# Performance work log

Measured on AMD Instinct MI355X. Metric: run time of the kernel, lower is better.

The kernel has to match this reference:

```python
import jax, jax.numpy as jnp
import numpy as np

AGENT_RADIUS = 0.2
SAFETY_DIST = 0.1
_ang = np.linspace(0.0, 2.0 * np.pi, 8, endpoint=False)
OBSTACLES = np.stack([10.0 * np.cos(_ang), 10.0 * np.sin(_ang), 0.5 * np.ones(8)], axis=-1).astype(np.float32)  # (x, y, r)


def _qp_solve(p, G, h):
    """Exact solve of: min_z 0.5 z^T z + p^T z  s.t. G z <= h, z in R^2.
    Equivalent to QPFunction with Q=I. Enumerates KKT candidates over active
    sets of size 0, 1, 2 (closed form in 2D) and picks the feasible optimum.
    p: [2], G: [m,2], h: [m]."""
    m = G.shape[0]
    ii, jj = np.triu_indices(m, 1)
    # active set {} -> unconstrained minimizer
    z0 = -p[None, :]                                        # [1,2]
    # active set {i}: z = -p - lam*g_i, g_i.z = h_i
    gg = jnp.sum(G * G, axis=-1)                            # [m]
    lam1 = (-(G @ p) - h) / (gg + 1e-12)
    z1 = -p[None, :] - lam1[:, None] * G                    # [m,2]
    ok1 = lam1 >= -1e-8
    # active set {i,j}: z solves 2x2 system [g_i; g_j] z = [h_i; h_j]
    Gi, Gj = G[ii], G[jj]                                   # [P,2]
    hi, hj = h[ii], h[jj]
    det = Gi[:, 0] * Gj[:, 1] - Gi[:, 1] * Gj[:, 0]
    det_ok = jnp.abs(det) > 1e-9
    ds = jnp.where(det_ok, det, 1.0)
    zx = (hi * Gj[:, 1] - hj * Gi[:, 1]) / ds
    zy = (Gi[:, 0] * hj - Gj[:, 0] * hi) / ds
    z2 = jnp.stack([zx, zy], axis=-1)                       # [P,2]
    r = -(z2 + p[None, :])                                  # A^T lam = r
    lam_i = (Gj[:, 1] * r[:, 0] - Gj[:, 0] * r[:, 1]) / ds
    lam_j = (Gi[:, 0] * r[:, 1] - Gi[:, 1] * r[:, 0]) / ds
    ok2 = det_ok & (lam_i >= -1e-8) & (lam_j >= -1e-8)
    Z = jnp.concatenate([z0, z1, z2], axis=0)               # [K,2]
    ok = jnp.concatenate([jnp.ones((1,), bool), ok1, ok2], axis=0)
    tol = 1e-6 * (1.0 + jnp.abs(h))
    feas = jnp.all(Z @ G.T <= (h + tol)[None, :], axis=-1)  # [K]
    obj = 0.5 * jnp.sum(Z * Z, axis=-1) + Z @ p
    obj = jnp.where(ok & feas, obj, jnp.inf)
    return Z[jnp.argmin(obj)]


def _forward(x, mean, std, W1, b1, W21, b21, W31, b31, W22, b22, W32, b32):
    x0 = x * std + mean                                     # de-normalized state [B,8]
    hid = jax.nn.relu(x @ W1.T + b1)
    x31 = jax.nn.relu(hid @ W21.T + b21) @ W31.T + b31      # reference control p [B,2]
    x32 = 4.0 * jax.nn.sigmoid(jax.nn.relu(hid @ W22.T + b22) @ W32.T + b32)  # CBF penalties [B,2]
    px, py, theta, v = x0[:, 0], x0[:, 1], x0[:, 2], x0[:, 3]
    ox, oy, oth, ov = x0[:, 4], x0[:, 5], x0[:, 6], x0[:, 7]
    st, ct = jnp.sin(theta), jnp.cos(theta)
    vs, vc = v * st, v * ct
    obs = jnp.asarray(OBSTACLES, x.dtype)
    # static obstacle constraints, vectorized over the n_obs obstacles
    dx = px[:, None] - obs[None, :, 0]                      # [B,n_obs]
    dy = py[:, None] - obs[None, :, 1]
    R = AGENT_RADIUS + obs[:, 2] + SAFETY_DIST
    bar = dx * dx + dy * dy - (R * R)[None, :]
    bdot = 2.0 * dx * vc[:, None] + 2.0 * dy * vs[:, None]
    Lf2b = (2.0 * v * v)[:, None]
    u1 = -2.0 * dx * vs[:, None] + 2.0 * dy * vc[:, None]
    u2 = 2.0 * dx * ct[:, None] + 2.0 * dy * st[:, None]
    G_obs = -jnp.stack([u1, u2], axis=-1)                   # [B,n_obs,2]
    s0, s1 = x32[:, 0:1], x32[:, 1:2]
    h_obs = Lf2b + (s0 + s1) * bdot + (s0 * s1) * bar       # [B,n_obs]
    # opponent constraint
    Ro = 2.0 * AGENT_RADIUS + SAFETY_DIST
    dxo, dyo = px - ox, py - oy
    so, co = jnp.sin(oth), jnp.cos(oth)
    bar_o = dxo * dxo + dyo * dyo - Ro * Ro
    bdot_o = 2.0 * dxo * (vc - ov * co) + 2.0 * dyo * (vs - ov * so)
    Lf2b_o = 2.0 * (v * v + ov * ov + 2.0 * v * ov * jnp.cos(theta - oth))
    u1o = -2.0 * dxo * vs + 2.0 * dyo * vc
    u2o = 2.0 * dxo * ct + 2.0 * dyo * st
    G_opp = -jnp.stack([u1o, u2o], axis=-1)[:, None, :]     # [B,1,2]
    h_opp = (Lf2b_o + (x32[:, 0] + x32[:, 1]) * bdot_o + x32[:, 0] * x32[:, 1] * bar_o)[:, None]
    G = jnp.concatenate([G_obs, G_opp], axis=1)             # [B,m,2]
    h = jnp.concatenate([h_obs, h_opp], axis=1)             # [B,m]
    return jax.vmap(_qp_solve)(x31, G, h)                   # [B,2]


def setup_inputs() -> dict:
    key = jax.random.key(0)
    ks = jax.random.split(key, 6)
    B, nF, H1, H2 = 65536, 8, 256, 128

    def lin(k, o, i):
        k1, k2 = jax.random.split(k)
        W = jax.random.normal(k1, (o, i), jnp.float32) / np.float32(np.sqrt(i))
        b = jax.random.normal(k2, (o,), jnp.float32) * 0.01
        return W, b

    W1, b1 = lin(ks[0], H1, nF)
    W21, b21 = lin(ks[1], H2, H1)
    W31, b31 = lin(ks[2], 2, H2)
    W22, b22 = lin(ks[3], H2, H1)
    W32, b32 = lin(ks[4], 2, H2)
    x = jax.random.normal(ks[5], (B, nF), jnp.float32)
    return {"x": x, "mean": jnp.zeros((nF,), jnp.float32), "std": jnp.ones((nF,), jnp.float32),
            "W1": W1, "b1": b1, "W21": W21, "b21": b21, "W31": W31, "b31": b31,
            "W22": W22, "b22": b22, "W32": W32, "b32": b32, "sgn": 1}


def reference(x, mean, std, W1, b1, W21, b21, W31, b31, W22, b22, W32, b32, sgn):
    # sgn==1 / training path -> batched differentiable QP solve
    return _forward(x, mean, std, W1, b1, W21, b21, W31, b31, W22, b22, W32, b32)
```

## Files before the change

### kernel.cpp

```cpp
#include <hip/hip_runtime.h>
#include <math.h>


typedef unsigned int u32;
typedef unsigned long long u64;
typedef unsigned short u16;
typedef __attribute__((ext_vector_type(8))) short short8;
typedef __attribute__((ext_vector_type(4))) float f32x4;
typedef __attribute__((ext_vector_type(2))) float f32x2;
typedef __attribute__((ext_vector_type(4))) u32 u32x4;

union Frag { short8 v; u32 u[4]; u32x4 q; };

__device__ __forceinline__ u16 f2bf(float f) {
    union { float f; u32 i; } v; v.f = f;
    u32 b = v.i;
    return (u16)((b + 0x7fffu + ((b >> 16) & 1u)) >> 16);
}
__device__ __forceinline__ u32 packbf(float a, float b) {
    return (u32)f2bf(a) | ((u32)f2bf(b) << 16);
}

__device__ const float OBX[8] = { 10.f, 7.07106781186547524f, 6.123234e-16f, -7.07106781186547524f,
                                 -10.f, -7.07106781186547524f, -1.8369702e-15f, 7.07106781186547524f };
__device__ const float OBY[8] = { 0.f, 7.07106781186547524f, 10.f, 7.07106781186547524f,
                                  1.2246468e-15f, -7.07106781186547524f, -10.f, -7.07106781186547524f };

#define PI0_ 0x2111111100000000ULL
#define PI1_ 0x5544443333322222ULL
#define PI2_ 0x7665ULL
#define PJ0_ 0x3876543287654321ULL
#define PJ1_ 0x7687658765487654ULL
#define PJ2_ 0x8878ULL
__device__ __forceinline__ int unpack4(u64 w0, u64 w1, u64 w2, int t) {
    u64 w = (t < 16) ? w0 : (t < 32) ? w1 : w2;
    return (int)((w >> ((t & 15) * 4)) & 15);
}

__global__ __launch_bounds__(256)
void prep_kernel(const float* __restrict__ W21, const float* __restrict__ W22,
                 u32* __restrict__ ws)
{
    int idx  = blockIdx.x * 256 + threadIdx.x;
    int lane = idx & 63;
    int nt   = (idx >> 6) & 7;
    int ks   = (idx >> 9) & 7;
    int head = idx >> 12;
    const float* W = head ? W22 : W21;
    int n  = nt * 16 + (lane & 15);
    int k0 = ks * 32 + (lane >> 4) * 8;
    const float* s = W + n * 256 + k0;
    u32x4 o;
    o.x = packbf(s[0], s[1]);
    o.y = packbf(s[2], s[3]);
    o.z = packbf(s[4], s[5]);
    o.w = packbf(s[6], s[7]);
    ((u32x4*)ws)[idx] = o;
}

__global__ __launch_bounds__(256)
void gemm_kernel(const float* __restrict__ x,
                 const float* __restrict__ W1,
                 const float* __restrict__ b1,
                 const float* __restrict__ b21,
                 const float* __restrict__ W31,
                 const float* __restrict__ b31,
                 const float* __restrict__ b22,
                 const float* __restrict__ W32,
                 const float* __restrict__ b32,
                 const u32* __restrict__ wsB,
                 f32x4* __restrict__ ps, int Btot)
{
    const int tid  = threadIdx.x;
    const int wave = tid >> 6;
    const int lane = tid & 63;
    const int q    = lane >> 4;
    const int m    = lane & 15;
    const int blockRow = blockIdx.x * 128;
    const int waveRow  = blockRow + wave * 32;

    __shared__ float lds_p[128][4];

    float xf0[8], xf1[8];
    {
        int R0 = waveRow + m, R1 = waveRow + 16 + m;
        const float* xp0 = x + (R0 < Btot ? R0 : 0) * 8;
        const float* xp1 = x + (R1 < Btot ? R1 : 0) * 8;
        #pragma unroll
        for (int c = 0; c < 8; ++c) { xf0[c] = xp0[c]; xf1[c] = xp1[c]; }
    }

    const f32x4* W1v = (const f32x4*)W1;
    const f32x4* b1v = (const f32x4*)b1;

    #pragma unroll 1
    for (int head = 0; head < 2; ++head) {
        const u32x4* Bb = (const u32x4*)wsB + head * 4096 + lane;
        const float* b2 = head ? b22 : b21;
        const float* W3 = head ? W32 : W31;
        const float* b3 = head ? b32 : b31;

        f32x4 acc[2][8];
        #pragma unroll
        for (int mt = 0; mt < 2; ++mt)
            #pragma unroll
            for (int nt = 0; nt < 8; ++nt) acc[mt][nt] = (f32x4){0.f, 0.f, 0.f, 0.f};

        #pragma unroll 1
        for (int ks = 0; ks < 8; ++ks) {
            int kb = ks * 32 + q * 8;
            f32x4 bA = b1v[kb >> 2];
            f32x4 bB = b1v[(kb >> 2) + 1];
            Frag A0, A1;
            float h0[8], h1[8];
            #pragma unroll
            for (int j = 0; j < 8; ++j) {
                f32x4 wa = W1v[(kb + j) * 2];
                f32x4 wb = W1v[(kb + j) * 2 + 1];
                float bj = (j < 4) ? bA[j] : bB[j - 4];
                float a0 = bj, a1 = bj;
                a0 = fmaf(wa.x, xf0[0], a0); a1 = fmaf(wa.x, xf1[0], a1);
                a0 = fmaf(wa.y, xf0[1], a0); a1 = fmaf(wa.y, xf1[1], a1);
                a0 = fmaf(wa.z, xf0[2], a0); a1 = fmaf(wa.z, xf1[2], a1);
                a0 = fmaf(wa.w, xf0[3], a0); a1 = fmaf(wa.w, xf1[3], a1);
                a0 = fmaf(wb.x, xf0[4], a0); a1 = fmaf(wb.x, xf1[4], a1);
                a0 = fmaf(wb.y, xf0[5], a0); a1 = fmaf(wb.y, xf1[5], a1);
                a0 = fmaf(wb.z, xf0[6], a0); a1 = fmaf(wb.z, xf1[6], a1);
                a0 = fmaf(wb.w, xf0[7], a0); a1 = fmaf(wb.w, xf1[7], a1);
                h0[j] = fmaxf(a0, 0.f);
                h1[j] = fmaxf(a1, 0.f);
            }
            #pragma unroll
            for (int t = 0; t < 4; ++t) {
                A0.u[t] = packbf(h0[2 * t], h0[2 * t + 1]);
                A1.u[t] = packbf(h1[2 * t], h1[2 * t + 1]);
            }
            const u32x4* Bks = Bb + ks * 512;
            #pragma unroll
            for (int nt = 0; nt < 8; ++nt) {
                Frag Bf; Bf.q = Bks[nt * 64];
                acc[0][nt] = __builtin_amdgcn_mfma_f32_16x16x32_bf16(A0.v, Bf.v, acc[0][nt], 0, 0, 0);
                acc[1][nt] = __builtin_amdgcn_mfma_f32_16x16x32_bf16(A1.v, Bf.v, acc[1][nt], 0, 0, 0);
            }
        }

        float pr0[2][4], pr1[2][4];
        #pragma unroll
        for (int mt = 0; mt < 2; ++mt)
            #pragma unroll
            for (int rg = 0; rg < 4; ++rg) { pr0[mt][rg] = 0.f; pr1[mt][rg] = 0.f; }
        #pragma unroll
        for (int nt = 0; nt < 8; ++nt) {
            int col = nt * 16 + m;
            float b2c = b2[col];
            float w0c = W3[col];
            float w1c = W3[128 + col];
            #pragma unroll
            for (int mt = 0; mt < 2; ++mt) {
                #pragma unroll
                for (int rg = 0; rg < 4; ++rg) {
                    float rv = fmaxf(acc[mt][nt][rg] + b2c, 0.f);
                    pr0[mt][rg] = fmaf(rv, w0c, pr0[mt][rg]);
                    pr1[mt][rg] = fmaf(rv, w1c, pr1[mt][rg]);
                }
            }
        }
        #pragma unroll
        for (int mt = 0; mt < 2; ++mt) {
            #pragma unroll
            for (int rg = 0; rg < 4; ++rg) {
                float v0 = pr0[mt][rg], v1 = pr1[mt][rg];
                #pragma unroll
                for (int off = 1; off < 16; off <<= 1) {
                    v0 += __shfl_xor(v0, off, 64);
                    v1 += __shfl_xor(v1, off, 64);
                }
                pr0[mt][rg] = v0; pr1[mt][rg] = v1;
            }
        }
        if (m == 0) {
            #pragma unroll
            for (int mt = 0; mt < 2; ++mt) {
                #pragma unroll
                for (int rg = 0; rg < 4; ++rg) {
                    int row = wave * 32 + mt * 16 + q * 4 + rg;
                    float a0 = pr0[mt][rg] + b3[0];
                    float a1 = pr1[mt][rg] + b3[1];
                    if (head == 0) {
                        lds_p[row][0] = a0;
                        lds_p[row][1] = a1;
                    } else {
                        lds_p[row][2] = 4.f / (1.f + expf(-a0));
                        lds_p[row][3] = 4.f / (1.f + expf(-a1));
                    }
                }
            }
        }
    }
    __syncthreads();

    if (tid < 128) {
        int R = blockRow + tid;
        if (R < Btot) ps[R] = *(const f32x4*)lds_p[tid];
    }
}

__global__ __launch_bounds__(256)
void qp_kernel(const float* __restrict__ x,
               const float* __restrict__ meanp,
               const float* __restrict__ stdp,
               const f32x4* __restrict__ ps,
               float* __restrict__ out, int Btot)
{
    const int tid  = threadIdx.x;
    const int rq   = tid & 127;
    const int half = tid >> 7;
    const int blockRow = blockIdx.x * 128;
    const int R    = blockRow + rq;

    __shared__ f32x4 qC[9][128];
    __shared__ f32x4 res[128];

    f32x4 pv = ps[R < Btot ? R : 0];
    float p0 = pv.x, p1 = pv.y;

    if (half == 0) {
        float s0 = pv.z, s1 = pv.w;
        float xr[8];
        const float* xp = x + (R < Btot ? R : 0) * 8;
        #pragma unroll
        for (int c = 0; c < 8; ++c) xr[c] = fmaf(xp[c], stdp[c], meanp[c]);
        float px = xr[0], py = xr[1], th = xr[2], v = xr[3];
        float ox = xr[4], oy = xr[5], oth = xr[6], ov = xr[7];
        float st = sinf(th),  ct = cosf(th);
        float so = sinf(oth), co = cosf(oth);
        float vs = v * st, vc = v * ct;
        float sps = s0 + s1, ss = s0 * s1;
        float Lf2b = 2.f * v * v;
        #pragma unroll 1
        for (int k = 0; k < 8; ++k) {
            float dx = px - OBX[k], dy = py - OBY[k];
            float bar  = dx * dx + dy * dy - 0.64f;
            float bdot = 2.f * dx * vc + 2.f * dy * vs;
            float gx = 2.f * dx * vs - 2.f * dy * vc;
            float gy = -(2.f * dx * ct + 2.f * dy * st);
            float hk = Lf2b + sps * bdot + ss * bar;
            float ht = hk + 1e-6f * (1.f + fabsf(hk));
            qC[k][rq] = (f32x4){gx, gy, hk, ht};
        }
        {
            float dxo = px - ox, dyo = py - oy;
            float bar_o  = dxo * dxo + dyo * dyo - 0.25f;
            float bdot_o = 2.f * dxo * (vc - ov * co) + 2.f * dyo * (vs - ov * so);
            float Lf2b_o = 2.f * (v * v + ov * ov + 2.f * v * ov * cosf(th - oth));
            float gx = 2.f * dxo * vs - 2.f * dyo * vc;
            float gy = -(2.f * dxo * ct + 2.f * dyo * st);
            float hk = Lf2b_o + sps * bdot_o + ss * bar_o;
            float ht = hk + 1e-6f * (1.f + fabsf(hk));
            qC[8][rq] = (f32x4){gx, gy, hk, ht};
        }
    }
    __syncthreads();

    const f32x4 C0 = qC[0][rq], C1 = qC[1][rq], C2 = qC[2][rq];
    const f32x4 C3 = qC[3][rq], C4 = qC[4][rq], C5 = qC[5][rq];
    const f32x4 C6 = qC[6][rq], C7 = qC[7][rq], C8 = qC[8][rq];

    const int c0i = half ? 23 : 0;
    const int c1i = half ? 46 : 23;
    float bobj = INFINITY;
    float bzx = -p0, bzy = -p1;
    #pragma unroll 2
    for (int c = c0i; c < c1i; ++c) {
        float zx, zy;
        bool pre;
        if (c == 0) {
            zx = -p0; zy = -p1; pre = true;
        } else if (c <= 9) {
            f32x4 g = qC[c - 1][rq];
            float gg  = g.x * g.x + g.y * g.y;
            float lam = (-(g.x * p0 + g.y * p1) - g.z) / (gg + 1e-12f);
            zx = -p0 - lam * g.x;
            zy = -p1 - lam * g.y;
            pre = (lam >= -1e-8f);
        } else {
            int t = c - 10;
            int pi = unpack4(PI0_, PI1_, PI2_, t);
            int pj = unpack4(PJ0_, PJ1_, PJ2_, t);
            f32x4 gi = qC[pi][rq];
            f32x4 gj = qC[pj][rq];
            float det = gi.x * gj.y - gi.y * gj.x;
            bool dok = fabsf(det) > 1e-9f;
            float ds = dok ? det : 1.0f;
            float inv = 1.0f / ds;
            zx = (gi.z * gj.y - gj.z * gi.y) * inv;
            zy = (gi.x * gj.z - gj.x * gi.z) * inv;
            float rx = -(zx + p0), ry = -(zy + p1);
            float li = (gj.y * rx - gj.x * ry) * inv;
            float lj = (gi.x * ry - gi.y * rx) * inv;
            pre = dok && (li >= -1e-8f) && (lj >= -1e-8f);
        }
        bool ok = pre;
        ok = ok && (zx * C0.x + zy * C0.y <= C0.w);
        ok = ok && (zx * C1.x + zy * C1.y <= C1.w);
        ok = ok && (zx * C2.x + zy * C2.y <= C2.w);
        ok = ok && (zx * C3.x + zy * C3.y <= C3.w);
        ok = ok && (zx * C4.x + zy * C4.y <= C4.w);
        ok = ok && (zx * C5.x + zy * C5.y <= C5.w);
        ok = ok && (zx * C6.x + zy * C6.y <= C6.w);
        ok = ok && (zx * C7.x + zy * C7.y <= C7.w);
        ok = ok && (zx * C8.x + zy * C8.y <= C8.w);
        float obj = 0.5f * (zx * zx + zy * zy) + zx * p0 + zy * p1;
        if (ok && obj < bobj) { bobj = obj; bzx = zx; bzy = zy; }
    }

    if (half) {
        res[rq] = (f32x4){bobj, bzx, bzy, 0.f};
    }
    __syncthreads();
    if (!half) {
        f32x4 r = res[rq];
        if (r.x < bobj) { bzx = r.y; bzy = r.z; }
        if (R < Btot) {
            f32x2 o2; o2.x = bzx; o2.y = bzy;
            ((f32x2*)out)[R] = o2;
        }
    }
}

extern "C" void kernel_launch(void* const* d_in, const int* in_sizes, int n_in,
                              void* d_out, int out_size, void* d_ws, size_t ws_size,
                              hipStream_t stream) {
    const float* x    = (const float*)d_in[0];
    const float* mean = (const float*)d_in[1];
    const float* stdv = (const float*)d_in[2];
    const float* W1   = (const float*)d_in[3];
    const float* b1   = (const float*)d_in[4];
    const float* W21  = (const float*)d_in[5];
    const float* b21  = (const float*)d_in[6];
    const float* W31  = (const float*)d_in[7];
    const float* b31  = (const float*)d_in[8];
    const float* W22  = (const float*)d_in[9];
    const float* b22  = (const float*)d_in[10];
    const float* W32  = (const float*)d_in[11];
    const float* b32  = (const float*)d_in[12];
    int B = in_sizes[0] / 8;
    float* out = (float*)d_out;
    u32* ws = (u32*)d_ws;
    f32x4* ps = (f32x4*)(ws + 32768);

    hipLaunchKernelGGL(prep_kernel, dim3(32), dim3(256), 0, stream, W21, W22, ws);

    int blocks = (B + 127) / 128;
    hipLaunchKernelGGL(gemm_kernel, dim3(blocks), dim3(256), 0, stream,
                       x, W1, b1, b21, W31, b31, b22, W32, b32, ws, ps, B);
    hipLaunchKernelGGL(qp_kernel, dim3(blocks), dim3(256), 0, stream,
                       x, mean, stdv, ps, out, B);
}
```

Baseline: 128.6 us.

## Fuse both MLP heads into one K loop sharing layer-1 activations

Merges the two head passes into a single K loop, so the first-layer hidden activations are computed and packed to bf16 once and feed MFMAs for both heads. This removes the duplicated layer-1 FMA work and W1 loads. In exchange the accumulator count doubles to 64 f32x4 per lane, which raises VGPR/AGPR pressure and may cut occupancy. It also swaps the hand-written bf16 rounding for the HIP packed conversion intrinsic.

```diff
diff --git a/kernel.cpp b/kernel.cpp
--- a/kernel.cpp
+++ b/kernel.cpp
@@ -1,4 +1,5 @@
 #include <hip/hip_runtime.h>
+#include <hip/hip_bf16.h>
 #include <math.h>
 
 
@@ -12,13 +13,11 @@
 
 union Frag { short8 v; u32 u[4]; u32x4 q; };
 
-__device__ __forceinline__ u16 f2bf(float f) {
-    union { float f; u32 i; } v; v.f = f;
-    u32 b = v.i;
-    return (u16)((b + 0x7fffu + ((b >> 16) & 1u)) >> 16);
-}
 __device__ __forceinline__ u32 packbf(float a, float b) {
-    return (u32)f2bf(a) | ((u32)f2bf(b) << 16);
+    float2 f2; f2.x = a; f2.y = b;
+    __hip_bfloat162 h = __float22bfloat162_rn(f2);
+    union { __hip_bfloat162 h2; u32 u; } cv; cv.h2 = h;
+    return cv.u;
 }
 
 __device__ const float OBX[8] = { 10.f, 7.07106781186547524f, 6.123234e-16f, -7.07106781186547524f,
@@ -93,57 +92,64 @@
     const f32x4* W1v = (const f32x4*)W1;
     const f32x4* b1v = (const f32x4*)b1;
 
+    f32x4 acc[2][2][8];
+    #pragma unroll
+    for (int hd = 0; hd < 2; ++hd)
+        #pragma unroll
+        for (int mt = 0; mt < 2; ++mt)
+            #pragma unroll
+            for (int nt = 0; nt < 8; ++nt) acc[hd][mt][nt] = (f32x4){0.f, 0.f, 0.f, 0.f};
+
+    const u32x4* Bb = (const u32x4*)wsB + lane;
+
     #pragma unroll 1
-    for (int head = 0; head < 2; ++head) {
-        const u32x4* Bb = (const u32x4*)wsB + head * 4096 + lane;
-        const float* b2 = head ? b22 : b21;
-        const float* W3 = head ? W32 : W31;
-        const float* b3 = head ? b32 : b31;
-
-        f32x4 acc[2][8];
-        #pragma unroll
-        for (int mt = 0; mt < 2; ++mt)
-            #pragma unroll
-            for (int nt = 0; nt < 8; ++nt) acc[mt][nt] = (f32x4){0.f, 0.f, 0.f, 0.f};
-
-        #pragma unroll 1
-        for (int ks = 0; ks < 8; ++ks) {
-            int kb = ks * 32 + q * 8;
-            f32x4 bA = b1v[kb >> 2];
-            f32x4 bB = b1v[(kb >> 2) + 1];
-            Frag A0, A1;
-            float h0[8], h1[8];
-            #pragma unroll
-            for (int j = 0; j < 8; ++j) {
-                f32x4 wa = W1v[(kb + j) * 2];
-                f32x4 wb = W1v[(kb + j) * 2 + 1];
-                float bj = (j < 4) ? bA[j] : bB[j - 4];
-                float a0 = bj, a1 = bj;
-                a0 = fmaf(wa.x, xf0[0], a0); a1 = fmaf(wa.x, xf1[0], a1);
-                a0 = fmaf(wa.y, xf0[1], a0); a1 = fmaf(wa.y, xf1[1], a1);
-                a0 = fmaf(wa.z, xf0[2], a0); a1 = fmaf(wa.z, xf1[2], a1);
-                a0 = fmaf(wa.w, xf0[3], a0); a1 = fmaf(wa.w, xf1[3], a1);
-                a0 = fmaf(wb.x, xf0[4], a0); a1 = fmaf(wb.x, xf1[4], a1);
-                a0 = fmaf(wb.y, xf0[5], a0); a1 = fmaf(wb.y, xf1[5], a1);
-                a0 = fmaf(wb.z, xf0[6], a0); a1 = fmaf(wb.z, xf1[6], a1);
-                a0 = fmaf(wb.w, xf0[7], a0); a1 = fmaf(wb.w, xf1[7], a1);
-                h0[j] = fmaxf(a0, 0.f);
-                h1[j] = fmaxf(a1, 0.f);
-            }
-            #pragma unroll
-            for (int t = 0; t < 4; ++t) {
-                A0.u[t] = packbf(h0[2 * t], h0[2 * t + 1]);
-                A1.u[t] = packbf(h1[2 * t], h1[2 * t + 1]);
-            }
-            const u32x4* Bks = Bb + ks * 512;
-            #pragma unroll
-            for (int nt = 0; nt < 8; ++nt) {
-                Frag Bf; Bf.q = Bks[nt * 64];
-                acc[0][nt] = __builtin_amdgcn_mfma_f32_16x16x32_bf16(A0.v, Bf.v, acc[0][nt], 0, 0, 0);
-                acc[1][nt] = __builtin_amdgcn_mfma_f32_16x16x32_bf16(A1.v, Bf.v, acc[1][nt], 0, 0, 0);
-            }
-        }
-
+    for (int ks = 0; ks < 8; ++ks) {
+        int kb = ks * 32 + q * 8;
+        f32x4 bA = b1v[kb >> 2];
+        f32x4 bB = b1v[(kb >> 2) + 1];
+        Frag A0, A1;
+        float h0[8], h1[8];
+        #pragma unroll
+        for (int j = 0; j < 8; ++j) {
+            f32x4 wa = W1v[(kb + j) * 2];
+            f32x4 wb = W1v[(kb + j) * 2 + 1];
+            float bj = (j < 4) ? bA[j] : bB[j - 4];
+            float a0 = bj, a1 = bj;
+            a0 = fmaf(wa.x, xf0[0], a0); a1 = fmaf(wa.x, xf1[0], a1);
+            a0 = fmaf(wa.y, xf0[1], a0); a1 = fmaf(wa.y, xf1[1], a1);
+            a0 = fmaf(wa.z, xf0[2], a0); a1 = fmaf(wa.z, xf1[2], a1);
+            a0 = fmaf(wa.w, xf0[3], a0); a1 = fmaf(wa.w, xf1[3], a1);
+            a0 = fmaf(wb.x, xf0[4], a0); a1 = fmaf(wb.x, xf1[4], a1);
+            a0 = fmaf(wb.y, xf0[5], a0); a1 = fmaf(wb.y, xf1[5], a1);
+            a0 = fmaf(wb.z, xf0[6], a0); a1 = fmaf(wb.z, xf1[6], a1);
+            a0 = fmaf(wb.w, xf0[7], a0); a1 = fmaf(wb.w, xf1[7], a1);
+            h0[j] = fmaxf(a0, 0.f);
+            h1[j] = fmaxf(a1, 0.f);
+        }
+        #pragma unroll
+        for (int t = 0; t < 4; ++t) {
+            A0.u[t] = packbf(h0[2 * t], h0[2 * t + 1]);
+            A1.u[t] = packbf(h1[2 * t], h1[2 * t + 1]);
+        }
+        const u32x4* Bks0 = Bb + ks * 512;
+        const u32x4* Bks1 = Bks0 + 4096;
+        #pragma unroll
+        for (int nt = 0; nt < 8; ++nt) {
+            Frag B0, B1;
+            B0.q = Bks0[nt * 64];
+            B1.q = Bks1[nt * 64];
+            acc[0][0][nt] = __builtin_amdgcn_mfma_f32_16x16x32_bf16(A0.v, B0.v, acc[0][0][nt], 0, 0, 0);
+            acc[0][1][nt] = __builtin_amdgcn_mfma_f32_16x16x32_bf16(A1.v, B0.v, acc[0][1][nt], 0, 0, 0);
+            acc[1][0][nt] = __builtin_amdgcn_mfma_f32_16x16x32_bf16(A0.v, B1.v, acc[1][0][nt], 0, 0, 0);
+            acc[1][1][nt] = __builtin_amdgcn_mfma_f32_16x16x32_bf16(A1.v, B1.v, acc[1][1][nt], 0, 0, 0);
+        }
+    }
+
+    #pragma unroll
+    for (int hd = 0; hd < 2; ++hd) {
+        const float* b2 = hd ? b22 : b21;
+        const float* W3 = hd ? W32 : W31;
+        const float* b3 = hd ? b32 : b31;
         float pr0[2][4], pr1[2][4];
         #pragma unroll
         for (int mt = 0; mt < 2; ++mt)
@@ -159,7 +165,7 @@
             for (int mt = 0; mt < 2; ++mt) {
                 #pragma unroll
                 for (int rg = 0; rg < 4; ++rg) {
-                    float rv = fmaxf(acc[mt][nt][rg] + b2c, 0.f);
+                    float rv = fmaxf(acc[hd][mt][nt][rg] + b2c, 0.f);
                     pr0[mt][rg] = fmaf(rv, w0c, pr0[mt][rg]);
                     pr1[mt][rg] = fmaf(rv, w1c, pr1[mt][rg]);
                 }
@@ -186,7 +192,7 @@
                     int row = wave * 32 + mt * 16 + q * 4 + rg;
                     float a0 = pr0[mt][rg] + b3[0];
                     float a1 = pr1[mt][rg] + b3[1];
-                    if (head == 0) {
+                    if (hd == 0) {
                         lds_p[row][0] = a0;
                         lds_p[row][1] = a1;
                     } else {
```

Result: slower. 141.1 us (+9.8%).

## Double-buffer B fragment loads across k-steps and vectorize x loads

Applied to the files above, without the earlier changes.

Prefetches the next k-step's weight fragments into registers (ping-pong Bc/Bn) while the current step computes layer-1 activations and runs MFMAs, so global load latency overlaps with compute. It also loads x rows as float4 vectors and swaps the manual bf16 rounding for the HIP intrinsic pair conversion. The cost is 64 extra VGPRs for the second fragment buffer, which may reduce occupancy, plus one redundant wrap-around prefetch per head.

```diff
diff --git a/kernel.cpp b/kernel.cpp
--- a/kernel.cpp
+++ b/kernel.cpp
@@ -1,4 +1,5 @@
 #include <hip/hip_runtime.h>
+#include <hip/hip_bf16.h>
 #include <math.h>
 
 
@@ -12,13 +13,11 @@
 
 union Frag { short8 v; u32 u[4]; u32x4 q; };
 
-__device__ __forceinline__ u16 f2bf(float f) {
-    union { float f; u32 i; } v; v.f = f;
-    u32 b = v.i;
-    return (u16)((b + 0x7fffu + ((b >> 16) & 1u)) >> 16);
-}
 __device__ __forceinline__ u32 packbf(float a, float b) {
-    return (u32)f2bf(a) | ((u32)f2bf(b) << 16);
+    float2 f2; f2.x = a; f2.y = b;
+    __hip_bfloat162 h = __float22bfloat162_rn(f2);
+    union { __hip_bfloat162 h2; u32 u; } cv; cv.h2 = h;
+    return cv.u;
 }
 
 __device__ const float OBX[8] = { 10.f, 7.07106781186547524f, 6.123234e-16f, -7.07106781186547524f,
@@ -56,6 +55,39 @@
     o.z = packbf(s[4], s[5]);
     o.w = packbf(s[6], s[7]);
     ((u32x4*)ws)[idx] = o;
+}
+
+__device__ __forceinline__ void layer1_pair(const f32x4* __restrict__ W1v,
+                                            const f32x4* __restrict__ b1v,
+                                            const f32x4& xa0, const f32x4& xb0,
+                                            const f32x4& xa1, const f32x4& xb1,
+                                            int kb, Frag& A0, Frag& A1)
+{
+    f32x4 bA = b1v[kb >> 2];
+    f32x4 bB = b1v[(kb >> 2) + 1];
+    float h0[8], h1[8];
+    #pragma unroll
+    for (int j = 0; j < 8; ++j) {
+        f32x4 wa = W1v[(kb + j) * 2];
+        f32x4 wb = W1v[(kb + j) * 2 + 1];
+        float bj = (j < 4) ? bA[j] : bB[j - 4];
+        float a0 = bj, a1 = bj;
+        a0 = fmaf(wa.x, xa0.x, a0); a1 = fmaf(wa.x, xa1.x, a1);
+        a0 = fmaf(wa.y, xa0.y, a0); a1 = fmaf(wa.y, xa1.y, a1);
+        a0 = fmaf(wa.z, xa0.z, a0); a1 = fmaf(wa.z, xa1.z, a1);
+        a0 = fmaf(wa.w, xa0.w, a0); a1 = fmaf(wa.w, xa1.w, a1);
+        a0 = fmaf(wb.x, xb0.x, a0); a1 = fmaf(wb.x, xb1.x, a1);
+        a0 = fmaf(wb.y, xb0.y, a0); a1 = fmaf(wb.y, xb1.y, a1);
+        a0 = fmaf(wb.z, xb0.z, a0); a1 = fmaf(wb.z, xb1.z, a1);
+        a0 = fmaf(wb.w, xb0.w, a0); a1 = fmaf(wb.w, xb1.w, a1);
+        h0[j] = fmaxf(a0, 0.f);
+        h1[j] = fmaxf(a1, 0.f);
+    }
+    #pragma unroll
+    for (int t = 0; t < 4; ++t) {
+        A0.u[t] = packbf(h0[2 * t], h0[2 * t + 1]);
+        A1.u[t] = packbf(h1[2 * t], h1[2 * t + 1]);
+    }
 }
 
 __global__ __launch_bounds__(256)
@@ -81,13 +113,13 @@
 
     __shared__ float lds_p[128][4];
 
-    float xf0[8], xf1[8];
+    f32x4 xa0, xb0, xa1, xb1;
     {
         int R0 = waveRow + m, R1 = waveRow + 16 + m;
-        const float* xp0 = x + (R0 < Btot ? R0 : 0) * 8;
-        const float* xp1 = x + (R1 < Btot ? R1 : 0) * 8;
-        #pragma unroll
-        for (int c = 0; c < 8; ++c) { xf0[c] = xp0[c]; xf1[c] = xp1[c]; }
+        const f32x4* xv0 = (const f32x4*)(x + (R0 < Btot ? R0 : 0) * 8);
+        const f32x4* xv1 = (const f32x4*)(x + (R1 < Btot ? R1 : 0) * 8);
+        xa0 = xv0[0]; xb0 = xv0[1];
+        xa1 = xv1[0]; xb1 = xv1[1];
     }
 
     const f32x4* W1v = (const f32x4*)W1;
@@ -106,41 +138,34 @@
             #pragma unroll
             for (int nt = 0; nt < 8; ++nt) acc[mt][nt] = (f32x4){0.f, 0.f, 0.f, 0.f};
 
+        Frag Bc[8], Bn[8];
+        #pragma unroll
+        for (int nt = 0; nt < 8; ++nt) Bc[nt].q = Bb[nt * 64];
+
         #pragma unroll 1
-        for (int ks = 0; ks < 8; ++ks) {
-            int kb = ks * 32 + q * 8;
-            f32x4 bA = b1v[kb >> 2];
-            f32x4 bB = b1v[(kb >> 2) + 1];
+        for (int ks = 0; ks < 8; ks += 2) {
+            {
+                const u32x4* Bp = Bb + (ks + 1) * 512;
+                #pragma unroll
+                for (int nt = 0; nt < 8; ++nt) Bn[nt].q = Bp[nt * 64];
+            }
             Frag A0, A1;
-            float h0[8], h1[8];
-            #pragma unroll
-            for (int j = 0; j < 8; ++j) {
-                f32x4 wa = W1v[(kb + j) * 2];
-                f32x4 wb = W1v[(kb + j) * 2 + 1];
-                float bj = (j < 4) ? bA[j] : bB[j - 4];
-                float a0 = bj, a1 = bj;
-                a0 = fmaf(wa.x, xf0[0], a0); a1 = fmaf(wa.x, xf1[0], a1);
-                a0 = fmaf(wa.y, xf0[1], a0); a1 = fmaf(wa.y, xf1[1], a1);
-                a0 = fmaf(wa.z, xf0[2], a0); a1 = fmaf(wa.z, xf1[2], a1);
-                a0 = fmaf(wa.w, xf0[3], a0); a1 = fmaf(wa.w, xf1[3], a1);
-                a0 = fmaf(wb.x, xf0[4], a0); a1 = fmaf(wb.x, xf1[4], a1);
-                a0 = fmaf(wb.y, xf0[5], a0); a1 = fmaf(wb.y, xf1[5], a1);
-                a0 = fmaf(wb.z, xf0[6], a0); a1 = fmaf(wb.z, xf1[6], a1);
-                a0 = fmaf(wb.w, xf0[7], a0); a1 = fmaf(wb.w, xf1[7], a1);
-                h0[j] = fmaxf(a0, 0.f);
-                h1[j] = fmaxf(a1, 0.f);
-            }
-            #pragma unroll
-            for (int t = 0; t < 4; ++t) {
-                A0.u[t] = packbf(h0[2 * t], h0[2 * t + 1]);
-                A1.u[t] = packbf(h1[2 * t], h1[2 * t + 1]);
-            }
-            const u32x4* Bks = Bb + ks * 512;
+            layer1_pair(W1v, b1v, xa0, xb0, xa1, xb1, ks * 32 + q * 8, A0, A1);
             #pragma unroll
             for (int nt = 0; nt < 8; ++nt) {
-                Frag Bf; Bf.q = Bks[nt * 64];
-                acc[0][nt] = __builtin_amdgcn_mfma_f32_16x16x32_bf16(A0.v, Bf.v, acc[0][nt], 0, 0, 0);
-                acc[1][nt] = __builtin_amdgcn_mfma_f32_16x16x32_bf16(A1.v, Bf.v, acc[1][nt], 0, 0, 0);
+                acc[0][nt] = __builtin_amdgcn_mfma_f32_16x16x32_bf16(A0.v, Bc[nt].v, acc[0][nt], 0, 0, 0);
+                acc[1][nt] = __builtin_amdgcn_mfma_f32_16x16x32_bf16(A1.v, Bc[nt].v, acc[1][nt], 0, 0, 0);
+            }
+            {
+                const u32x4* Bp = Bb + ((ks + 2) & 7) * 512;
+                #pragma unroll
+                for (int nt = 0; nt < 8; ++nt) Bc[nt].q = Bp[nt * 64];
+            }
+            layer1_pair(W1v, b1v, xa0, xb0, xa1, xb1, (ks + 1) * 32 + q * 8, A0, A1);
+            #pragma unroll
+            for (int nt = 0; nt < 8; ++nt) {
+                acc[0][nt] = __builtin_amdgcn_mfma_f32_16x16x32_bf16(A0.v, Bn[nt].v, acc[0][nt], 0, 0, 0);
+                acc[1][nt] = __builtin_amdgcn_mfma_f32_16x16x32_bf16(A1.v, Bn[nt].v, acc[1][nt], 0, 0, 0);
             }
         }
 
```

Result: slower. 144.5 us (+12.4%).
